# Kernel tuning notes

Hardware: AMD Instinct MI355X
Metric: run time of the kernel (lower is better)

Reference implementation:

```python
import jax, jax.numpy as jnp
import numpy as np

EPS = 1e-8

def prelu(x, a):
    return jnp.where(x >= 0, x, a * x)

def setup_inputs() -> dict:
    key = jax.random.key(0)
    ks = jax.random.split(key, 8)
    B, G, N, T = 4, 8, 128, 6000
    H = 384
    x = jax.random.normal(ks[0], (B, G, N, T), dtype=jnp.float32)
    # torch.nn.Linear default init: U(-1/sqrt(fan_in), 1/sqrt(fan_in))
    def lin(k, out_f, in_f):
        k1, k2 = jax.random.split(k)
        bound = 1.0 / np.sqrt(in_f)
        W = jax.random.uniform(k1, (out_f, in_f), minval=-bound, maxval=bound, dtype=jnp.float32)
        b = jax.random.uniform(k2, (out_f,), minval=-bound, maxval=bound, dtype=jnp.float32)
        return W, b
    Wi, bi = lin(ks[1], H, N)
    Wm, bm = lin(ks[2], H, H)
    Wo, bo = lin(ks[3], N, 2 * H)
    # PReLU default: single learnable scalar initialized to 0.25
    ai = jnp.float32(0.25)
    am = jnp.float32(0.25)
    ao = jnp.float32(0.25)
    gamma = jnp.ones((N,), dtype=jnp.float32)
    beta = jnp.zeros((N,), dtype=jnp.float32)
    return {"input": x, "Wi": Wi, "bi": bi, "ai": ai, "Wm": Wm, "bm": bm, "am": am,
            "Wo": Wo, "bo": bo, "ao": ao, "gamma": gamma, "beta": beta}

def reference(input, Wi, bi, ai, Wm, bm, am, Wo, bo, ao, gamma, beta):
    B, G, N, T = input.shape
    # [B, T, G, N]
    h = jnp.transpose(input, (0, 3, 1, 2))
    # TAC_input: Linear(N->H) + PReLU
    gi = prelu(jnp.einsum('btgn,hn->btgh', h, Wi) + bi, ai)          # [B,T,G,H]
    # mean over groups, TAC_mean: Linear(H->H) + PReLU
    gm = gi.mean(axis=2)                                              # [B,T,H]
    gm = prelu(jnp.einsum('bth,oh->bto', gm, Wm) + bm, am)            # [B,T,H]
    gm = jnp.broadcast_to(gm[:, :, None, :], gi.shape)                # [B,T,G,H]
    cat = jnp.concatenate([gi, gm], axis=-1)                          # [B,T,G,2H]
    # TAC_output: Linear(2H->N) + PReLU
    go = prelu(jnp.einsum('btgc,nc->btgn', cat, Wo) + bo, ao)         # [B,T,G,N]
    go = jnp.transpose(go, (0, 2, 3, 1))                              # [B,G,N,T]
    # GlobLN over (N, T) per (batch*G) sample, affine along channel N
    mean = go.mean(axis=(2, 3), keepdims=True)
    var = jnp.mean((go - mean) ** 2, axis=(2, 3), keepdims=True)
    normed = (go - mean) / jnp.sqrt(var + EPS)
    go = gamma[None, None, :, None] * normed + beta[None, None, :, None]
    return input + go
```

## Files before the change

kernel.cpp:

```cpp
#include <hip/hip_runtime.h>

typedef __bf16 bf16_t;
typedef __bf16 bf16x8 __attribute__((ext_vector_type(8)));
typedef float f32x4 __attribute__((ext_vector_type(4)));

static constexpr int Bq = 4, Gg = 8, Nn = 128, Tt = 6000, Hh = 384;
static constexpr int TB = 16;
static constexpr int NTPB = Tt / TB;
static constexpr int NTILES = Bq * NTPB;
static constexpr int LDA = 136;
static constexpr int LDG = 392;
static constexpr int LDSM = 392;
static constexpr int LDV = 132;

static constexpr size_t OFF_WI  = 0;
static constexpr size_t OFF_WM  = OFF_WI + (size_t)Hh * Nn * 2;
static constexpr size_t OFF_WO  = OFF_WM + (size_t)Hh * Hh * 2;
static constexpr size_t OFF_PT  = OFF_WO + (size_t)Nn * 2 * Hh * 2;
static constexpr size_t OFF_MRS = OFF_PT + (size_t)NTILES * 8 * 16 * 4;
static constexpr size_t OFF_GO  = (size_t)2 << 20;
static constexpr size_t WS_NEED = OFF_GO + (size_t)Bq * Tt * Gg * Nn * 2;

static constexpr int SM_GI = 0;
static constexpr int SM_SM = 100352;
static constexpr int SM_AS = 112896;
static constexpr int SM_MM = 112896;
static constexpr int SM_VV = 112896 + 12544;
static constexpr int SMEM_BYTES = 147712;

#define MFMA16(a, b, c) __builtin_amdgcn_mfma_f32_16x16x32_bf16((a), (b), (c), 0, 0, 0)

__global__ void k0_prep(const float* __restrict__ Wi, const float* __restrict__ Wm,
                        const float* __restrict__ Wo,
                        bf16_t* __restrict__ WiB, bf16_t* __restrict__ WmB,
                        bf16_t* __restrict__ WoB) {
    int i = blockIdx.x * blockDim.x + threadIdx.x;
    const int n1 = Hh * Nn, n2 = Hh * Hh, n3 = Nn * 2 * Hh;
    for (int idx = i; idx < n1 + n2 + n3; idx += gridDim.x * blockDim.x) {
        if (idx < n1)            WiB[idx] = (bf16_t)Wi[idx];
        else if (idx < n1 + n2)  WmB[idx - n1] = (bf16_t)Wm[idx - n1];
        else                     WoB[idx - n1 - n2] = (bf16_t)Wo[idx - n1 - n2];
    }
}

__device__ __forceinline__ int as_col(int row, int c) {
    return ((((c >> 3) ^ ((row >> 3) & 7)) << 3) | (c & 7));
}

__global__ __launch_bounds__(512, 1)
void k1_fused(const float* __restrict__ x,
              const bf16_t* __restrict__ WiB, const float* __restrict__ bi, const float* __restrict__ aip,
              const bf16_t* __restrict__ WmB, const float* __restrict__ bm, const float* __restrict__ amp,
              const bf16_t* __restrict__ WoB, const float* __restrict__ bo, const float* __restrict__ aop,
              bf16_t* __restrict__ go, float* __restrict__ part) {
    __shared__ char smem[SMEM_BYTES];
    bf16_t* Gi = (bf16_t*)(smem + SM_GI);
    bf16_t* Sm = (bf16_t*)(smem + SM_SM);
    bf16_t* As = (bf16_t*)(smem + SM_AS);
    bf16_t* Mm = (bf16_t*)(smem + SM_MM);
    float*  Vv = (float*)(smem + SM_VV);

    const int tid  = threadIdx.x;
    const int lane = tid & 63;
    const int w    = tid >> 6;
    const int l15  = lane & 15;
    const int l4   = lane >> 4;
    const int tile = blockIdx.x;
    const int b    = tile / NTPB, t0 = (tile % NTPB) * TB;

    {
        const int g0 = tid >> 7, n0 = tid & 127;
        #pragma unroll
        for (int h = 0; h < 2; h++) {
            int gg = g0 + 4 * h;
            #pragma unroll
            for (int q = 0; q < 4; q++) {
                f32x4 xv = *(const f32x4*)&x[((size_t)((b * Gg + gg) * Nn + n0)) * Tt + t0 + 4 * q];
                #pragma unroll
                for (int e = 0; e < 4; e++) {
                    int row = (q * 4 + e) * Gg + gg;
                    As[row * LDA + as_col(row, n0)] = (bf16_t)xv[e];
                }
            }
        }
    }
    __syncthreads();

    const float ai = aip[0], am = amp[0], ao = aop[0];

    {
        const int cb = w * 48;
        f32x4 acc[8][3];
        #pragma unroll
        for (int mt = 0; mt < 8; mt++)
            #pragma unroll
            for (int nc = 0; nc < 3; nc++) acc[mt][nc] = f32x4{0.f, 0.f, 0.f, 0.f};
        #pragma unroll
        for (int kk = 0; kk < 4; kk++) {
            const int k0 = kk * 32 + l4 * 8;
            bf16x8 bb[3];
            #pragma unroll
            for (int nc = 0; nc < 3; nc++)
                bb[nc] = *(const bf16x8*)&WiB[(cb + nc * 16 + l15) * Nn + k0];
            #pragma unroll
            for (int mt = 0; mt < 8; mt++) {
                int row = mt * 16 + l15;
                bf16x8 a = *(const bf16x8*)&As[row * LDA + as_col(row, k0)];
                #pragma unroll
                for (int nc = 0; nc < 3; nc++) acc[mt][nc] = MFMA16(a, bb[nc], acc[mt][nc]);
            }
        }
        #pragma unroll
        for (int nc = 0; nc < 3; nc++) {
            int col = cb + nc * 16 + l15;
            float bv = bi[col];
            #pragma unroll
            for (int mt = 0; mt < 8; mt++) {
                float ms = 0.f;
                #pragma unroll
                for (int j = 0; j < 4; j++) {
                    int row = mt * 16 + l4 * 4 + j;
                    float v = acc[mt][nc][j] + bv;
                    v = v >= 0.f ? v : ai * v;
                    Gi[row * LDG + col] = (bf16_t)v;
                    ms += v;
                }
                ms += __shfl_xor(ms, 16, 64);
                if ((l4 & 1) == 0) {
                    int tl = mt * 2 + (l4 >> 1);
                    Sm[tl * LDSM + col] = (bf16_t)(0.125f * ms);
                }
            }
        }
    }
    __syncthreads();

    {
        const int cb2 = w * 48;
        f32x4 acc2[3];
        #pragma unroll
        for (int nc = 0; nc < 3; nc++) acc2[nc] = f32x4{0.f, 0.f, 0.f, 0.f};
        #pragma unroll
        for (int kk = 0; kk < 12; kk++) {
            const int k0 = kk * 32 + l4 * 8;
            bf16x8 a = *(const bf16x8*)&Sm[l15 * LDSM + k0];
            #pragma unroll
            for (int nc = 0; nc < 3; nc++) {
                bf16x8 bb = *(const bf16x8*)&WmB[(cb2 + nc * 16 + l15) * Hh + k0];
                acc2[nc] = MFMA16(a, bb, acc2[nc]);
            }
        }
        #pragma unroll
        for (int nc = 0; nc < 3; nc++) {
            int col = cb2 + nc * 16 + l15;
            float bv = bm[col];
            #pragma unroll
            for (int j = 0; j < 4; j++) {
                float v = acc2[nc][j] + bv;
                v = v >= 0.f ? v : am * v;
                Mm[(l4 * 4 + j) * LDSM + col] = (bf16_t)v;
            }
        }
    }
    __syncthreads();

    {
        const int nblk = w * 16;
        f32x4 acc3 = f32x4{0.f, 0.f, 0.f, 0.f};
        #pragma unroll
        for (int kk = 0; kk < 12; kk++) {
            const int k0 = kk * 32 + l4 * 8;
            bf16x8 a = *(const bf16x8*)&Mm[l15 * LDSM + k0];
            bf16x8 bb = *(const bf16x8*)&WoB[(nblk + l15) * 768 + 384 + k0];
            acc3 = MFMA16(a, bb, acc3);
        }
        #pragma unroll
        for (int j = 0; j < 4; j++) Vv[(l4 * 4 + j) * LDV + nblk + l15] = acc3[j];
    }

    const int mh = w >> 2, ws4 = w & 3;
    const int cb4 = ws4 * 32;
    f32x4 acc4[4][2];
    #pragma unroll
    for (int mt = 0; mt < 4; mt++)
        #pragma unroll
        for (int nc = 0; nc < 2; nc++) acc4[mt][nc] = f32x4{0.f, 0.f, 0.f, 0.f};
    #pragma unroll
    for (int kk = 0; kk < 12; kk++) {
        const int k0 = kk * 32 + l4 * 8;
        bf16x8 b0 = *(const bf16x8*)&WoB[(cb4 + l15) * 768 + k0];
        bf16x8 b1 = *(const bf16x8*)&WoB[(cb4 + 16 + l15) * 768 + k0];
        bf16x8 a[4];
        #pragma unroll
        for (int mt = 0; mt < 4; mt++)
            a[mt] = *(const bf16x8*)&Gi[(mh * 64 + mt * 16 + l15) * LDG + k0];
        #pragma unroll
        for (int mt = 0; mt < 4; mt++) {
            acc4[mt][0] = MFMA16(a[mt], b0, acc4[mt][0]);
            acc4[mt][1] = MFMA16(a[mt], b1, acc4[mt][1]);
        }
    }
    __syncthreads();

    {
        float gsum[4] = {0.f, 0.f, 0.f, 0.f};
        float gss[4]  = {0.f, 0.f, 0.f, 0.f};
        #pragma unroll
        for (int nc = 0; nc < 2; nc++) {
            int col = cb4 + nc * 16 + l15;
            float bv = bo[col];
            #pragma unroll
            for (int mt = 0; mt < 4; mt++) {
                #pragma unroll
                for (int j = 0; j < 4; j++) {
                    int row = mh * 64 + mt * 16 + l4 * 4 + j;
                    int tl = row >> 3;
                    int g = row & 7;
                    float v = acc4[mt][nc][j] + Vv[tl * LDV + col] + bv;
                    v = v >= 0.f ? v : ao * v;
                    go[((size_t)((b * Tt + t0 + tl) * Gg + g)) * Nn + col] = (bf16_t)v;
                    gsum[j] += v;
                    gss[j] += v * v;
                }
            }
        }
        #pragma unroll
        for (int j = 0; j < 4; j++) {
            float s = gsum[j], q = gss[j];
            #pragma unroll
            for (int off = 1; off < 16; off <<= 1) {
                s += __shfl_xor(s, off, 64);
                q += __shfl_xor(q, off, 64);
            }
            s += __shfl_xor(s, 32, 64);
            q += __shfl_xor(q, 32, 64);
            if (l15 == 0 && l4 < 2) {
                int g = l4 * 4 + j;
                part[((size_t)tile * 8 + w) * 16 + g * 2 + 0] = s;
                part[((size_t)tile * 8 + w) * 16 + g * 2 + 1] = q;
            }
        }
    }
}

__global__ __launch_bounds__(1024)
void k_final(const float* __restrict__ part, float* __restrict__ mr) {
    __shared__ float red[64][17];
    const int tid = threadIdx.x, key = tid & 63, chunk = tid >> 6;
    const int bb = key >> 4;
    const int rowsPerB = NTPB * 8;
    const int t0 = chunk * 188;
    const int cnt = min(188, rowsPerB - t0);
    float s = 0.f;
    for (int i = 0; i < cnt; i++)
        s += part[(size_t)(bb * rowsPerB + t0 + i) * 16 + (key & 15)];
    red[key][chunk] = s;
    __syncthreads();
    if (tid < 64) {
        float tot = 0.f;
        #pragma unroll
        for (int ch = 0; ch < 16; ch++) tot += red[tid][ch];
        red[tid][16] = tot;
    }
    __syncthreads();
    if (tid < 32) {
        int b2 = tid >> 3, g2 = tid & 7;
        float s0 = red[b2 * 16 + g2 * 2][16];
        float s1 = red[b2 * 16 + g2 * 2 + 1][16];
        const float cntf = (float)Nn * (float)Tt;
        float mean = s0 / cntf;
        float var = s1 / cntf - mean * mean;
        mr[tid * 2] = mean;
        mr[tid * 2 + 1] = rsqrtf(var + 1e-8f);
    }
}

__global__ __launch_bounds__(256)
void k_apply(const float* __restrict__ x, const bf16_t* __restrict__ go,
             const float* __restrict__ mr, const float* __restrict__ gamma,
             const float* __restrict__ beta, float* __restrict__ out) {
    __shared__ float tr[32][65];
    int bid = blockIdx.x;
    const int tt = bid % 94; bid /= 94;
    const int nn = bid & 3;  bid >>= 2;
    const int g = bid & 7;
    const int b = bid >> 3;
    const int t0 = tt * 64, n0 = nn * 32;
    const int tid = threadIdx.x;
    const float mean = mr[(b * 8 + g) * 2], rstd = mr[(b * 8 + g) * 2 + 1];

    for (int idx = tid; idx < 2048; idx += 256) {
        int nl = idx & 31, tl = idx >> 5;
        int t = t0 + tl;
        float v = 0.f;
        if (t < Tt) v = (float)go[((size_t)((b * Tt + t) * Gg + g)) * Nn + n0 + nl];
        tr[nl][tl] = v;
    }
    __syncthreads();
    for (int idx = tid; idx < 2048; idx += 256) {
        int tl = idx & 63, nl = idx >> 6;
        int t = t0 + tl;
        if (t < Tt) {
            int n = n0 + nl;
            size_t a = ((size_t)((b * Gg + g) * Nn + n)) * Tt + t;
            out[a] = x[a] + gamma[n] * (tr[nl][tl] - mean) * rstd + beta[n];
        }
    }
}

extern "C" void kernel_launch(void* const* d_in, const int* in_sizes, int n_in,
                              void* d_out, int out_size, void* d_ws, size_t ws_size,
                              hipStream_t stream) {
    const float* x     = (const float*)d_in[0];
    const float* Wi    = (const float*)d_in[1];
    const float* bi    = (const float*)d_in[2];
    const float* ai    = (const float*)d_in[3];
    const float* Wm    = (const float*)d_in[4];
    const float* bm    = (const float*)d_in[5];
    const float* am    = (const float*)d_in[6];
    const float* Wo    = (const float*)d_in[7];
    const float* bo    = (const float*)d_in[8];
    const float* ao    = (const float*)d_in[9];
    const float* gamma = (const float*)d_in[10];
    const float* beta  = (const float*)d_in[11];
    float* out = (float*)d_out;
    char* ws = (char*)d_ws;

    if (ws_size < WS_NEED) return;

    bf16_t* WiB = (bf16_t*)(ws + OFF_WI);
    bf16_t* WmB = (bf16_t*)(ws + OFF_WM);
    bf16_t* WoB = (bf16_t*)(ws + OFF_WO);
    float*  prt = (float*)(ws + OFF_PT);
    float*  mrs = (float*)(ws + OFF_MRS);
    bf16_t* goB = (bf16_t*)(ws + OFF_GO);

    k0_prep<<<dim3(512), dim3(256), 0, stream>>>(Wi, Wm, Wo, WiB, WmB, WoB);
    k1_fused<<<dim3(NTILES), dim3(512), 0, stream>>>(
        x, WiB, bi, ai, WmB, bm, am, WoB, bo, ao, goB, prt);
    k_final<<<dim3(1), dim3(1024), 0, stream>>>(prt, mrs);
    k_apply<<<dim3(Bq * Gg * 4 * 94), dim3(256), 0, stream>>>(x, goB, mrs, gamma, beta, out);
}
```

Measured before the change: 294.5 us.

## Fuse input projection into output GEMM per warp, shrink LDS for higher occupancy

Each warp now owns 16 rows and computes the Wi projection in 32-column chunks, writing them to a small double-buffered LDS scratch and feeding them straight into the Wo GEMM. This removes the full 128x384 Gi buffer, so shared memory drops from about 148KB to about 68KB and launch bounds allow 4 blocks per CU. The per-warp GlobLN partials are combined in LDS with atomics into one row per tile, and k_final is rewritten to match. In exchange, each warp now re-reads all of the Wi and Wo weights from global memory or cache, instead of sharing weight tiles across warps.

```diff
diff --git a/kernel.cpp b/kernel.cpp
--- a/kernel.cpp
+++ b/kernel.cpp
@@ -9,7 +9,6 @@
 static constexpr int NTPB = Tt / TB;
 static constexpr int NTILES = Bq * NTPB;
 static constexpr int LDA = 136;
-static constexpr int LDG = 392;
 static constexpr int LDSM = 392;
 static constexpr int LDV = 132;
 
@@ -17,16 +16,16 @@
 static constexpr size_t OFF_WM  = OFF_WI + (size_t)Hh * Nn * 2;
 static constexpr size_t OFF_WO  = OFF_WM + (size_t)Hh * Hh * 2;
 static constexpr size_t OFF_PT  = OFF_WO + (size_t)Nn * 2 * Hh * 2;
-static constexpr size_t OFF_MRS = OFF_PT + (size_t)NTILES * 8 * 16 * 4;
+static constexpr size_t OFF_MRS = OFF_PT + (size_t)NTILES * 16 * 4;
 static constexpr size_t OFF_GO  = (size_t)2 << 20;
 static constexpr size_t WS_NEED = OFF_GO + (size_t)Bq * Tt * Gg * Nn * 2;
 
-static constexpr int SM_GI = 0;
-static constexpr int SM_SM = 100352;
-static constexpr int SM_AS = 112896;
-static constexpr int SM_MM = 112896;
-static constexpr int SM_VV = 112896 + 12544;
-static constexpr int SMEM_BYTES = 147712;
+static constexpr int SM_AS = 0;
+static constexpr int SM_SM = 34816;
+static constexpr int SM_MM = 47360;
+static constexpr int SM_VV = 59904;
+static constexpr int SM_ST = 68352;
+static constexpr int SMEM_BYTES = 68416;
 
 #define MFMA16(a, b, c) __builtin_amdgcn_mfma_f32_16x16x32_bf16((a), (b), (c), 0, 0, 0)
 
@@ -47,18 +46,18 @@
     return ((((c >> 3) ^ ((row >> 3) & 7)) << 3) | (c & 7));
 }
 
-__global__ __launch_bounds__(512, 1)
+__global__ __launch_bounds__(512, 4)
 void k1_fused(const float* __restrict__ x,
               const bf16_t* __restrict__ WiB, const float* __restrict__ bi, const float* __restrict__ aip,
               const bf16_t* __restrict__ WmB, const float* __restrict__ bm, const float* __restrict__ amp,
               const bf16_t* __restrict__ WoB, const float* __restrict__ bo, const float* __restrict__ aop,
               bf16_t* __restrict__ go, float* __restrict__ part) {
     __shared__ char smem[SMEM_BYTES];
-    bf16_t* Gi = (bf16_t*)(smem + SM_GI);
+    bf16_t* As = (bf16_t*)(smem + SM_AS);
     bf16_t* Sm = (bf16_t*)(smem + SM_SM);
-    bf16_t* As = (bf16_t*)(smem + SM_AS);
     bf16_t* Mm = (bf16_t*)(smem + SM_MM);
     float*  Vv = (float*)(smem + SM_VV);
+    float*  st = (float*)(smem + SM_ST);
 
     const int tid  = threadIdx.x;
     const int lane = tid & 63;
@@ -68,6 +67,8 @@
     const int tile = blockIdx.x;
     const int b    = tile / NTPB, t0 = (tile % NTPB) * TB;
 
+    if (tid < 16) st[tid] = 0.f;
+
     {
         const int g0 = tid >> 7, n0 = tid & 127;
         #pragma unroll
@@ -88,49 +89,48 @@
 
     const float ai = aip[0], am = amp[0], ao = aop[0];
 
-    {
-        const int cb = w * 48;
-        f32x4 acc[8][3];
-        #pragma unroll
-        for (int mt = 0; mt < 8; mt++)
-            #pragma unroll
-            for (int nc = 0; nc < 3; nc++) acc[mt][nc] = f32x4{0.f, 0.f, 0.f, 0.f};
-        #pragma unroll
-        for (int kk = 0; kk < 4; kk++) {
-            const int k0 = kk * 32 + l4 * 8;
-            bf16x8 bb[3];
-            #pragma unroll
-            for (int nc = 0; nc < 3; nc++)
-                bb[nc] = *(const bf16x8*)&WiB[(cb + nc * 16 + l15) * Nn + k0];
-            #pragma unroll
-            for (int mt = 0; mt < 8; mt++) {
-                int row = mt * 16 + l15;
-                bf16x8 a = *(const bf16x8*)&As[row * LDA + as_col(row, k0)];
-                #pragma unroll
-                for (int nc = 0; nc < 3; nc++) acc[mt][nc] = MFMA16(a, bb[nc], acc[mt][nc]);
-            }
-        }
-        #pragma unroll
-        for (int nc = 0; nc < 3; nc++) {
-            int col = cb + nc * 16 + l15;
-            float bv = bi[col];
-            #pragma unroll
-            for (int mt = 0; mt < 8; mt++) {
-                float ms = 0.f;
-                #pragma unroll
-                for (int j = 0; j < 4; j++) {
-                    int row = mt * 16 + l4 * 4 + j;
-                    float v = acc[mt][nc][j] + bv;
-                    v = v >= 0.f ? v : ai * v;
-                    Gi[row * LDG + col] = (bf16_t)v;
-                    ms += v;
-                }
-                ms += __shfl_xor(ms, 16, 64);
-                if ((l4 & 1) == 0) {
-                    int tl = mt * 2 + (l4 >> 1);
-                    Sm[tl * LDSM + col] = (bf16_t)(0.125f * ms);
-                }
-            }
+    const int row = w * 16 + l15;
+    bf16x8 af[4];
+    #pragma unroll
+    for (int kk = 0; kk < 4; kk++)
+        af[kk] = *(const bf16x8*)&As[row * LDA + as_col(row, kk * 32 + l4 * 8)];
+
+    bf16_t* scr = As + w * 16 * LDA;
+    f32x4 acc4[8];
+    #pragma unroll
+    for (int nf = 0; nf < 8; nf++) acc4[nf] = f32x4{0.f, 0.f, 0.f, 0.f};
+
+    #pragma unroll 2
+    for (int q = 0; q < 12; q++) {
+        bf16_t* scrq = scr + (q & 1) * 640;
+        #pragma unroll
+        for (int half = 0; half < 2; half++) {
+            const int nc = q * 2 + half;
+            f32x4 a1 = f32x4{0.f, 0.f, 0.f, 0.f};
+            #pragma unroll
+            for (int kk = 0; kk < 4; kk++) {
+                bf16x8 bb = *(const bf16x8*)&WiB[(nc * 16 + l15) * Nn + kk * 32 + l4 * 8];
+                a1 = MFMA16(af[kk], bb, a1);
+            }
+            const int col = nc * 16 + l15;
+            const float bv = bi[col];
+            float ms = 0.f;
+            #pragma unroll
+            for (int j = 0; j < 4; j++) {
+                float v = a1[j] + bv;
+                v = v >= 0.f ? v : ai * v;
+                scrq[(l4 * 4 + j) * 40 + half * 16 + l15] = (bf16_t)v;
+                ms += v;
+            }
+            ms += __shfl_xor(ms, 16, 64);
+            if ((l4 & 1) == 0)
+                Sm[(2 * w + (l4 >> 1)) * LDSM + col] = (bf16_t)(0.125f * ms);
+        }
+        bf16x8 at = *(const bf16x8*)&scrq[l15 * 40 + l4 * 8];
+        #pragma unroll
+        for (int nf = 0; nf < 8; nf++) {
+            bf16x8 bw = *(const bf16x8*)&WoB[(nf * 16 + l15) * 768 + q * 32 + l4 * 8];
+            acc4[nf] = MFMA16(at, bw, acc4[nf]);
         }
     }
     __syncthreads();
@@ -177,51 +177,25 @@
         #pragma unroll
         for (int j = 0; j < 4; j++) Vv[(l4 * 4 + j) * LDV + nblk + l15] = acc3[j];
     }
-
-    const int mh = w >> 2, ws4 = w & 3;
-    const int cb4 = ws4 * 32;
-    f32x4 acc4[4][2];
-    #pragma unroll
-    for (int mt = 0; mt < 4; mt++)
-        #pragma unroll
-        for (int nc = 0; nc < 2; nc++) acc4[mt][nc] = f32x4{0.f, 0.f, 0.f, 0.f};
-    #pragma unroll
-    for (int kk = 0; kk < 12; kk++) {
-        const int k0 = kk * 32 + l4 * 8;
-        bf16x8 b0 = *(const bf16x8*)&WoB[(cb4 + l15) * 768 + k0];
-        bf16x8 b1 = *(const bf16x8*)&WoB[(cb4 + 16 + l15) * 768 + k0];
-        bf16x8 a[4];
-        #pragma unroll
-        for (int mt = 0; mt < 4; mt++)
-            a[mt] = *(const bf16x8*)&Gi[(mh * 64 + mt * 16 + l15) * LDG + k0];
-        #pragma unroll
-        for (int mt = 0; mt < 4; mt++) {
-            acc4[mt][0] = MFMA16(a[mt], b0, acc4[mt][0]);
-            acc4[mt][1] = MFMA16(a[mt], b1, acc4[mt][1]);
-        }
-    }
     __syncthreads();
 
     {
         float gsum[4] = {0.f, 0.f, 0.f, 0.f};
         float gss[4]  = {0.f, 0.f, 0.f, 0.f};
         #pragma unroll
-        for (int nc = 0; nc < 2; nc++) {
-            int col = cb4 + nc * 16 + l15;
+        for (int nf = 0; nf < 8; nf++) {
+            int col = nf * 16 + l15;
             float bv = bo[col];
             #pragma unroll
-            for (int mt = 0; mt < 4; mt++) {
-                #pragma unroll
-                for (int j = 0; j < 4; j++) {
-                    int row = mh * 64 + mt * 16 + l4 * 4 + j;
-                    int tl = row >> 3;
-                    int g = row & 7;
-                    float v = acc4[mt][nc][j] + Vv[tl * LDV + col] + bv;
-                    v = v >= 0.f ? v : ao * v;
-                    go[((size_t)((b * Tt + t0 + tl) * Gg + g)) * Nn + col] = (bf16_t)v;
-                    gsum[j] += v;
-                    gss[j] += v * v;
-                }
+            for (int j = 0; j < 4; j++) {
+                int rl = l4 * 4 + j;
+                int tl = 2 * w + (rl >> 3);
+                int g = rl & 7;
+                float v = acc4[nf][j] + Vv[tl * LDV + col] + bv;
+                v = v >= 0.f ? v : ao * v;
+                go[((size_t)((b * Tt + t0 + tl) * Gg + g)) * Nn + col] = (bf16_t)v;
+                gsum[j] += v;
+                gss[j] += v * v;
             }
         }
         #pragma unroll
@@ -236,37 +210,40 @@
             q += __shfl_xor(q, 32, 64);
             if (l15 == 0 && l4 < 2) {
                 int g = l4 * 4 + j;
-                part[((size_t)tile * 8 + w) * 16 + g * 2 + 0] = s;
-                part[((size_t)tile * 8 + w) * 16 + g * 2 + 1] = q;
-            }
-        }
-    }
+                atomicAdd(&st[g * 2 + 0], s);
+                atomicAdd(&st[g * 2 + 1], q);
+            }
+        }
+    }
+    __syncthreads();
+    if (tid < 16) part[(size_t)tile * 16 + tid] = st[tid];
 }
 
 __global__ __launch_bounds__(1024)
 void k_final(const float* __restrict__ part, float* __restrict__ mr) {
-    __shared__ float red[64][17];
-    const int tid = threadIdx.x, key = tid & 63, chunk = tid >> 6;
-    const int bb = key >> 4;
-    const int rowsPerB = NTPB * 8;
-    const int t0 = chunk * 188;
-    const int cnt = min(188, rowsPerB - t0);
-    float s = 0.f;
-    for (int i = 0; i < cnt; i++)
-        s += part[(size_t)(bb * rowsPerB + t0 + i) * 16 + (key & 15)];
-    red[key][chunk] = s;
-    __syncthreads();
-    if (tid < 64) {
-        float tot = 0.f;
-        #pragma unroll
-        for (int ch = 0; ch < 16; ch++) tot += red[tid][ch];
-        red[tid][16] = tot;
-    }
-    __syncthreads();
+    __shared__ float red[64][16];
+    __shared__ float tot[4][16];
+    const int tid = threadIdx.x;
+    const int col = tid & 15, rb = tid >> 4;
+    float s[4] = {0.f, 0.f, 0.f, 0.f};
+    for (int k = 0; k < 24; k++) {
+        int row = rb + (k << 6);
+        if (row < NTILES) s[row / NTPB] += part[(size_t)row * 16 + col];
+    }
+    for (int b2 = 0; b2 < 4; b2++) {
+        red[rb][col] = s[b2];
+        __syncthreads();
+        if (tid < 16) {
+            float t = 0.f;
+            #pragma unroll 8
+            for (int r = 0; r < 64; r++) t += red[r][tid];
+            tot[b2][tid] = t;
+        }
+        __syncthreads();
+    }
     if (tid < 32) {
         int b2 = tid >> 3, g2 = tid & 7;
-        float s0 = red[b2 * 16 + g2 * 2][16];
-        float s1 = red[b2 * 16 + g2 * 2 + 1][16];
+        float s0 = tot[b2][g2 * 2], s1 = tot[b2][g2 * 2 + 1];
         const float cntf = (float)Nn * (float)Tt;
         float mean = s0 / cntf;
         float var = s1 / cntf - mean * mean;
```

Result: slower. 405.7 us (+37.8%).
